# Kernel optimization log

Hardware: AMD Instinct MI355X
Metric: run time of the kernel (lower is better)

The kernel has to match this reference:

```python
import jax, jax.numpy as jnp
import numpy as np

def setup_inputs() -> dict:
    key = jax.random.key(0)
    k1, k2, k3, k4 = jax.random.split(key, 4)
    B, S, E, H = 4, 4096, 1024, 64
    x = jax.random.normal(k1, (B, S, E), dtype=jnp.float32)
    scale = E ** -0.5  # keep activations well-scaled like trained Linear weights
    Wq = jax.random.normal(k2, (E, H), dtype=jnp.float32) * scale
    Wk = jax.random.normal(k3, (E, H), dtype=jnp.float32) * scale
    Wv = jax.random.normal(k4, (E, H), dtype=jnp.float32) * scale
    return {"x": x, "Wq": Wq, "Wk": Wk, "Wv": Wv}

def reference(x, Wq, Wk, Wv):
    # x: [B, S, E]; W*: [E, H]
    B, S, E = x.shape
    H = Wq.shape[1]
    q = jnp.einsum('bse,eh->bsh', x, Wq)
    k = jnp.einsum('bse,eh->bsh', x, Wk)
    v = jnp.einsum('bse,eh->bsh', x, Wv)
    att = jnp.einsum('bqh,bkh->bqk', q, k) * (H ** -0.5)  # [B, S, S]
    causal = jnp.tril(jnp.ones((S, S), dtype=bool))
    att = jnp.where(causal, att, -jnp.inf)
    att = jax.nn.softmax(att, axis=-1)
    # dropout p=0.0 (eval-mode): identity
    return jnp.einsum('bqk,bkh->bqh', att, v)
```

## Files before the change

### kernel.cpp

```cpp
#include <hip/hip_runtime.h>


using short8 = __attribute__((ext_vector_type(8))) short;
using f32x4  = __attribute__((ext_vector_type(4))) float;

#define MFMA16(A, B, C) __builtin_amdgcn_mfma_f32_16x16x32_bf16((A), (B), (C), 0, 0, 0)

typedef const __attribute__((address_space(1))) void* gas_ptr;
typedef __attribute__((address_space(3))) void*       las_ptr;

__device__ __forceinline__ void gload16(const void* g, void* l) {
    __builtin_amdgcn_global_load_lds((gas_ptr)g, (las_ptr)l, 16, 0, 0);
}

__device__ __forceinline__ unsigned short f2bf(float f) {
    unsigned u = __builtin_bit_cast(unsigned, f);
    u += 0x7fffu + ((u >> 16) & 1u);
    return (unsigned short)(u >> 16);
}
__device__ __forceinline__ float bf2f(unsigned short u) {
    unsigned v = ((unsigned)u) << 16;
    return __builtin_bit_cast(float, v);
}

__device__ __forceinline__ float exp2_fast(float x) {
#if __has_builtin(__builtin_amdgcn_exp2f)
    return __builtin_amdgcn_exp2f(x);
#else
    float r;
    asm("v_exp_f32 %0, %1" : "=v"(r) : "v"(x));
    return r;
#endif
}

__global__ __launch_bounds__(256) void transpose_w(
    const float* __restrict__ Wq,
    const float* __restrict__ Wk,
    const float* __restrict__ Wv,
    unsigned short* __restrict__ Ws)
{
    int o = blockIdx.x * 256 + threadIdx.x;
    if (o < 196608) {
        int j    = o & 7;
        int l    = (o >> 3) & 63;
        int g    = (o >> 9) & 7;
        int rem  = o >> 12;
        int mt   = rem % 3;
        int sk   = rem / 3;
        int c    = g >> 2, nt = g & 3;
        int quad = l >> 4, n  = l & 15;
        int e    = sk * 64 + c * 32 + quad * 8 + j;
        int h    = nt * 16 + n;
        const float* W = (mt == 0) ? Wq : (mt == 1) ? Wk : Wv;
        Ws[o] = f2bf(W[e * 64 + h]);
    }
}

__global__ __launch_bounds__(256, 3) void proj_all(
    const float* __restrict__ x,
    const unsigned short* __restrict__ Ws,
    unsigned short* __restrict__ Qo,
    unsigned short* __restrict__ Ko,
    unsigned short* __restrict__ Vto)
{
    const int m0   = blockIdx.x * 32;
    const int tid  = threadIdx.x;
    const int lane = tid & 63;
    const int ch   = tid >> 6;
    const int quad = lane >> 4;
    const int n    = lane & 15;

    __shared__ __align__(16) float xs[2][8][64][4];

    const f32x4 zero4 = {0.f, 0.f, 0.f, 0.f};
    f32x4 acc[3][2];
    #pragma unroll
    for (int mt = 0; mt < 3; ++mt)
        #pragma unroll
        for (int rg = 0; rg < 2; ++rg) acc[mt][rg] = zero4;

    auto stage = [&](int t, int p) {
        int k0 = t * 64;
        #pragma unroll
        for (int it = 0; it < 2; ++it) {
            int i     = ch + 4 * it;
            int chunk = n ^ (quad << 2);
            gload16(x + (size_t)(m0 + 4 * i + quad) * 1024 + k0 + chunk * 4,
                    &xs[p][i][0][0]);
        }
    };

    stage(0, 0);
    __syncthreads();

    int p = 0;
    for (int t = 0; t < 16; ++t) {
        if (t < 15) stage(t + 1, p ^ 1);

        const unsigned short* wp = Ws + (((size_t)t * 24) << 9) + (size_t)lane * 8;
        short8 w0[3], w1[3];
        #pragma unroll
        for (int mt = 0; mt < 3; ++mt) {
            w0[mt] = *(const short8*)(wp + ((size_t)(mt * 8 + ch)     << 9));
            w1[mt] = *(const short8*)(wp + ((size_t)(mt * 8 + 4 + ch) << 9));
        }

        #pragma unroll
        for (int rg = 0; rg < 2; ++rg) {
            int sub = n & 3, s = sub << 2;
            const float* xp = &xs[p][rg * 4 + (n >> 2)][0][0] + sub * 64;
            f32x4 u0 = *(const f32x4*)(xp + (((2 * quad)     ^ s) << 2));
            f32x4 u1 = *(const f32x4*)(xp + (((2 * quad + 1) ^ s) << 2));
            f32x4 u2 = *(const f32x4*)(xp + (((8 + 2 * quad) ^ s) << 2));
            f32x4 u3 = *(const f32x4*)(xp + (((9 + 2 * quad) ^ s) << 2));
            short8 a0, a1;
            #pragma unroll
            for (int j = 0; j < 4; ++j) {
                a0[j]     = (short)f2bf(u0[j]);
                a0[4 + j] = (short)f2bf(u1[j]);
                a1[j]     = (short)f2bf(u2[j]);
                a1[4 + j] = (short)f2bf(u3[j]);
            }
            #pragma unroll
            for (int mt = 0; mt < 3; ++mt) {
                acc[mt][rg] = MFMA16(a0, w0[mt], acc[mt][rg]);
                acc[mt][rg] = MFMA16(a1, w1[mt], acc[mt][rg]);
            }
        }

        __syncthreads();
        p ^= 1;
    }

    const int h = ch * 16 + n;
    #pragma unroll
    for (int rg = 0; rg < 2; ++rg) {
        #pragma unroll
        for (int r = 0; r < 4; ++r) {
            int m = m0 + rg * 16 + quad * 4 + r;
            Qo[(size_t)m * 64 + h] = f2bf(acc[0][rg][r]);
            Ko[(size_t)m * 64 + h] = f2bf(acc[1][rg][r]);
            int b = m >> 12, s2 = m & 4095;
            Vto[((size_t)(b * 80 + h)) * 4096 + s2] = f2bf(acc[2][rg][r]);
        }
    }
}

template <int SPLIT>
__device__ __forceinline__ void attn_body(
    const unsigned short* __restrict__ Q,
    const unsigned short* __restrict__ K,
    const unsigned short* __restrict__ Vt,
    float* __restrict__ dst,
    int b, int r0, int kt0, int kt1)
{
    const int tid  = threadIdx.x;
    const int lane = tid & 63;
    const int wv   = tid >> 6;
    const int quad = lane >> 4;
    const int n    = lane & 15;
    const int ktmask = r0 >> 6;

    __shared__ __align__(16) short kf[2][8][64][8];
    __shared__ __align__(16) short vf[2][8][64][8];
    __shared__ __align__(16) unsigned short pbuf[4][32][72];

    short8 qa[2][2];
    #pragma unroll
    for (int rg = 0; rg < 2; ++rg) {
        const unsigned short* qp =
            Q + (size_t)(b * 4096 + r0 + wv * 32 + rg * 16 + n) * 64 + quad * 8;
        #pragma unroll
        for (int j = 0; j < 8; ++j) {
            qa[rg][0][j] = (short)f2bf(bf2f(qp[j])      * 0.18033688f);
            qa[rg][1][j] = (short)f2bf(bf2f(qp[32 + j]) * 0.18033688f);
        }
    }

    const f32x4 zero4 = {0.f, 0.f, 0.f, 0.f};
    f32x4 oacc[2][4];
    float lacc[2][4];
    #pragma unroll
    for (int rg = 0; rg < 2; ++rg)
        #pragma unroll
        for (int nt = 0; nt < 4; ++nt) { oacc[rg][nt] = zero4; lacc[rg][nt] = 0.f; }

    const unsigned short* kbase = K  + ((size_t)b * 4096 + n) * 64 + quad * 8;
    const unsigned short* vbase = Vt + ((size_t)b * 80 + n) * 4096 + quad * 8;

    auto stage = [&](int kt, int p) {
        #pragma unroll
        for (int it = 0; it < 4; ++it) {
            int f = wv + 4 * it;
            if (f < 8) {
                int c = f >> 2, nt = f & 3;
                gload16(kbase + (size_t)(kt * 64 + nt * 16) * 64 + c * 32, &kf[p][f][0][0]);
            } else {
                int pnl = f - 8;
                int nt = pnl >> 1, c = pnl & 1;
                gload16(vbase + (size_t)nt * 16 * 4096 + kt * 64 + c * 32, &vf[p][pnl][0][0]);
            }
        }
    };

    int p = 0;
    stage(kt0, 0);
    __syncthreads();

    for (int kt = kt0; kt <= kt1; ++kt) {
        if (kt < kt1) stage(kt + 1, p ^ 1);

        f32x4 sacc[2][4];
        #pragma unroll
        for (int rg = 0; rg < 2; ++rg)
            #pragma unroll
            for (int nt = 0; nt < 4; ++nt) sacc[rg][nt] = zero4;

        #pragma unroll
        for (int nt = 0; nt < 4; ++nt) {
            short8 ka = *(const short8*)(&kf[p][nt][lane][0]);
            short8 kb = *(const short8*)(&kf[p][4 + nt][lane][0]);
            #pragma unroll
            for (int rg = 0; rg < 2; ++rg) {
                sacc[rg][nt] = MFMA16(qa[rg][0], ka, sacc[rg][nt]);
                sacc[rg][nt] = MFMA16(qa[rg][1], kb, sacc[rg][nt]);
            }
        }

        if (kt >= ktmask) {
            #pragma unroll
            for (int rg = 0; rg < 2; ++rg) {
                int qg = r0 + wv * 32 + rg * 16 + quad * 4;
                #pragma unroll
                for (int nt = 0; nt < 4; ++nt)
                    #pragma unroll
                    for (int r = 0; r < 4; ++r) {
                        int key = kt * 64 + nt * 16 + n;
                        if (key > qg + r) sacc[rg][nt][r] = -1e30f;
                    }
            }
        }

        #pragma unroll
        for (int rg = 0; rg < 2; ++rg)
            #pragma unroll
            for (int r = 0; r < 4; ++r) {
                float rs = 0.f;
                #pragma unroll
                for (int nt = 0; nt < 4; ++nt) {
                    unsigned short pv = f2bf(exp2_fast(sacc[rg][nt][r]));
                    pbuf[wv][rg * 16 + quad * 4 + r][nt * 16 + n] = pv;
                    rs += bf2f(pv);
                }
                lacc[rg][r] += rs;
            }

        short8 pa[2][2];
        #pragma unroll
        for (int rg = 0; rg < 2; ++rg) {
            pa[rg][0] = *(const short8*)(&pbuf[wv][rg * 16 + n][quad * 8]);
            pa[rg][1] = *(const short8*)(&pbuf[wv][rg * 16 + n][32 + quad * 8]);
        }
        #pragma unroll
        for (int nt = 0; nt < 4; ++nt) {
            short8 va = *(const short8*)(&vf[p][2 * nt][lane][0]);
            short8 vb = *(const short8*)(&vf[p][2 * nt + 1][lane][0]);
            #pragma unroll
            for (int rg = 0; rg < 2; ++rg) {
                oacc[rg][nt] = MFMA16(pa[rg][0], va, oacc[rg][nt]);
                oacc[rg][nt] = MFMA16(pa[rg][1], vb, oacc[rg][nt]);
            }
        }

        __syncthreads();
        p ^= 1;
    }

    #pragma unroll
    for (int rg = 0; rg < 2; ++rg)
        #pragma unroll
        for (int r = 0; r < 4; ++r) {
            float v = lacc[rg][r];
            v += __shfl_xor(v, 1);
            v += __shfl_xor(v, 2);
            v += __shfl_xor(v, 4);
            v += __shfl_xor(v, 8);
            lacc[rg][r] = v;
        }

    if (SPLIT) {
        #pragma unroll
        for (int rg = 0; rg < 2; ++rg)
            #pragma unroll
            for (int r = 0; r < 4; ++r) {
                int row = wv * 32 + rg * 16 + quad * 4 + r;
                #pragma unroll
                for (int nt = 0; nt < 4; ++nt)
                    dst[row * 64 + nt * 16 + n] = oacc[rg][nt][r];
                if (n == 0) dst[8192 + row] = lacc[rg][r];
            }
    } else {
        #pragma unroll
        for (int rg = 0; rg < 2; ++rg)
            #pragma unroll
            for (int r = 0; r < 4; ++r) {
                float inv = 1.f / lacc[rg][r];
                int q = r0 + wv * 32 + rg * 16 + quad * 4 + r;
                #pragma unroll
                for (int nt = 0; nt < 4; ++nt)
                    dst[(size_t)(b * 4096 + q) * 64 + nt * 16 + n] = oacc[rg][nt][r] * inv;
            }
    }
}

__global__ __launch_bounds__(256, 3) void attn_part(
    const unsigned short* __restrict__ Q,
    const unsigned short* __restrict__ K,
    const unsigned short* __restrict__ Vt,
    float* __restrict__ Part)
{
    int id = blockIdx.x;
    int b  = id & 3;
    int t  = 143 - (id >> 2);
    int g  = 0;
    while (2 * (g + 1) * (g + 2) <= t) ++g;
    int u  = t - 2 * g * (g + 1);
    int qt = 4 * g + u / (g + 1);
    int c  = u - (u / (g + 1)) * (g + 1);

    int r0  = qt * 128;
    int kt0 = c * 8;
    int kt1 = min(kt0 + 7, 2 * qt + 1);

    float* dst = Part + (size_t)(b * 144 + t) * 8320;
    attn_body<1>(Q, K, Vt, dst, b, r0, kt0, kt1);
}

__global__ __launch_bounds__(256, 3) void attn_mono(
    const unsigned short* __restrict__ Q,
    const unsigned short* __restrict__ K,
    const unsigned short* __restrict__ Vt,
    float* __restrict__ out)
{
    int id = blockIdx.x;
    int qt = 31 - (id >> 2);
    int b  = id & 3;
    attn_body<0>(Q, K, Vt, out, b, qt * 128, 0, 2 * qt + 1);
}

__global__ __launch_bounds__(256) void combine(
    const float* __restrict__ Part, float* __restrict__ out)
{
    int id    = blockIdx.x;
    int slice = id & 7;
    int bq    = id >> 3;
    int b     = bq & 3;
    int qt    = bq >> 2;
    int g     = qt >> 2;
    int nc    = g + 1;
    int t0    = 2 * g * (g + 1) + (qt & 3) * (g + 1);
    const float* P0 = Part + (size_t)(b * 144 + t0) * 8320;

    int tid = threadIdx.x;

    __shared__ float invden[16];
    if (tid < 16) {
        float d[8] = {0, 0, 0, 0, 0, 0, 0, 0};
        #pragma unroll 8
        for (int c = 0; c < 8; ++c)
            if (c < nc) d[c] = P0[c * 8320 + 8192 + slice * 16 + tid];
        invden[tid] = 1.f / (((d[0] + d[1]) + (d[2] + d[3])) +
                             ((d[4] + d[5]) + (d[6] + d[7])));
    }

    float acc[4] = {0, 0, 0, 0};
    const float* Pe = P0 + slice * 1024 + tid;
    for (int c = 0; c < nc; ++c) {
        const float* Pc = Pe + (size_t)c * 8320;
        #pragma unroll
        for (int j = 0; j < 4; ++j)
            acc[j] += Pc[j * 256];
    }

    __syncthreads();
    #pragma unroll
    for (int j = 0; j < 4; ++j) {
        int e   = j * 256 + tid;
        int row = e >> 6;
        out[((size_t)b * 4096 + qt * 128 + slice * 16) * 64 + (size_t)e]
            = acc[j] * invden[row];
    }
}

extern "C" void kernel_launch(void* const* d_in, const int* in_sizes, int n_in,
                              void* d_out, int out_size, void* d_ws, size_t ws_size,
                              hipStream_t stream) {
    const float* x  = (const float*)d_in[0];
    const float* Wq = (const float*)d_in[1];
    const float* Wk = (const float*)d_in[2];
    const float* Wv = (const float*)d_in[3];
    float* outp = (float*)d_out;
    unsigned short* ws = (unsigned short*)d_ws;

    unsigned short* Qw  = ws;
    unsigned short* Kw  = ws + 1048576;
    unsigned short* Vtw = ws + 2097152;
    unsigned short* Wsp = ws + 3407872;

    size_t part_off = ((size_t)3604480 * 2 + 255) & ~(size_t)255;
    size_t need     = part_off + (size_t)4 * 144 * 8320 * 4;
    float* Part = (float*)((char*)d_ws + part_off);

    transpose_w<<<dim3(768), dim3(256), 0, stream>>>(Wq, Wk, Wv, Wsp);
    proj_all<<<dim3(512), dim3(256), 0, stream>>>(x, Wsp, Qw, Kw, Vtw);

    if (ws_size >= need) {
        attn_part<<<dim3(576), dim3(256), 0, stream>>>(Qw, Kw, Vtw, Part);
        combine<<<dim3(1024), dim3(256), 0, stream>>>(Part, outp);
    } else {
        attn_mono<<<dim3(128), dim3(256), 0, stream>>>(Qw, Kw, Vtw, outp);
    }
}
```

Measured before the change: 141.8 us.

## Load x directly into registers in projection, dropping LDS staging and barriers

The projection kernel no longer stages x tiles through shared memory with async global-to-LDS loads and per-iteration __syncthreads. Each lane now loads its own fp32 x fragments straight into registers, double-buffered across a fully unrolled K loop, with a sched_barrier to order loads ahead of compute. This removes LDS traffic and block synchronization but raises register pressure and may give less coalesced global access. Separately, the attention softmax row sum now accumulates the fp32 exponentials rather than the bf16-rounded values, which saves one conversion per element but slightly changes numerics.

```diff
diff --git a/kernel.cpp b/kernel.cpp
--- a/kernel.cpp
+++ b/kernel.cpp
@@ -70,8 +70,6 @@
     const int quad = lane >> 4;
     const int n    = lane & 15;
 
-    __shared__ __align__(16) float xs[2][8][64][4];
-
     const f32x4 zero4 = {0.f, 0.f, 0.f, 0.f};
     f32x4 acc[3][2];
     #pragma unroll
@@ -79,47 +77,40 @@
         #pragma unroll
         for (int rg = 0; rg < 2; ++rg) acc[mt][rg] = zero4;
 
-    auto stage = [&](int t, int p) {
-        int k0 = t * 64;
-        #pragma unroll
-        for (int it = 0; it < 2; ++it) {
-            int i     = ch + 4 * it;
-            int chunk = n ^ (quad << 2);
-            gload16(x + (size_t)(m0 + 4 * i + quad) * 1024 + k0 + chunk * 4,
-                    &xs[p][i][0][0]);
-        }
+    const float* xr0 = x + (size_t)(m0 + n) * 1024 + 8 * quad;
+    const float* xr1 = x + (size_t)(m0 + 16 + n) * 1024 + 8 * quad;
+    const unsigned short* wl = Ws + (size_t)lane * 8;
+
+    auto xload = [&](int t, f32x4 (&u)[2][4]) {
+        const float* p0 = xr0 + t * 64;
+        const float* p1 = xr1 + t * 64;
+        u[0][0] = *(const f32x4*)(p0);
+        u[0][1] = *(const f32x4*)(p0 + 4);
+        u[0][2] = *(const f32x4*)(p0 + 32);
+        u[0][3] = *(const f32x4*)(p0 + 36);
+        u[1][0] = *(const f32x4*)(p1);
+        u[1][1] = *(const f32x4*)(p1 + 4);
+        u[1][2] = *(const f32x4*)(p1 + 32);
+        u[1][3] = *(const f32x4*)(p1 + 36);
     };
-
-    stage(0, 0);
-    __syncthreads();
-
-    int p = 0;
-    for (int t = 0; t < 16; ++t) {
-        if (t < 15) stage(t + 1, p ^ 1);
-
-        const unsigned short* wp = Ws + (((size_t)t * 24) << 9) + (size_t)lane * 8;
-        short8 w0[3], w1[3];
+    auto wload = [&](int t, short8 (&w0)[3], short8 (&w1)[3]) {
+        const unsigned short* wp = wl + (((size_t)t * 24) << 9);
         #pragma unroll
         for (int mt = 0; mt < 3; ++mt) {
             w0[mt] = *(const short8*)(wp + ((size_t)(mt * 8 + ch)     << 9));
             w1[mt] = *(const short8*)(wp + ((size_t)(mt * 8 + 4 + ch) << 9));
         }
-
+    };
+    auto compute = [&](f32x4 (&u)[2][4], short8 (&w0)[3], short8 (&w1)[3]) {
         #pragma unroll
         for (int rg = 0; rg < 2; ++rg) {
-            int sub = n & 3, s = sub << 2;
-            const float* xp = &xs[p][rg * 4 + (n >> 2)][0][0] + sub * 64;
-            f32x4 u0 = *(const f32x4*)(xp + (((2 * quad)     ^ s) << 2));
-            f32x4 u1 = *(const f32x4*)(xp + (((2 * quad + 1) ^ s) << 2));
-            f32x4 u2 = *(const f32x4*)(xp + (((8 + 2 * quad) ^ s) << 2));
-            f32x4 u3 = *(const f32x4*)(xp + (((9 + 2 * quad) ^ s) << 2));
             short8 a0, a1;
             #pragma unroll
             for (int j = 0; j < 4; ++j) {
-                a0[j]     = (short)f2bf(u0[j]);
-                a0[4 + j] = (short)f2bf(u1[j]);
-                a1[j]     = (short)f2bf(u2[j]);
-                a1[4 + j] = (short)f2bf(u3[j]);
+                a0[j]     = (short)f2bf(u[rg][0][j]);
+                a0[4 + j] = (short)f2bf(u[rg][1][j]);
+                a1[j]     = (short)f2bf(u[rg][2][j]);
+                a1[4 + j] = (short)f2bf(u[rg][3][j]);
             }
             #pragma unroll
             for (int mt = 0; mt < 3; ++mt) {
@@ -127,9 +118,20 @@
                 acc[mt][rg] = MFMA16(a1, w1[mt], acc[mt][rg]);
             }
         }
-
-        __syncthreads();
-        p ^= 1;
+    };
+
+    f32x4 uA[2][4], uB[2][4];
+    short8 w0[3], w1[3];
+    xload(0, uA);
+
+    #pragma unroll
+    for (int t = 0; t < 16; ++t) {
+        wload(t, w0, w1);
+        if (t < 15) {
+            if (t & 1) xload(t + 1, uA); else xload(t + 1, uB);
+        }
+        __builtin_amdgcn_sched_barrier(0);
+        if (t & 1) compute(uB, w0, w1); else compute(uA, w0, w1);
     }
 
     const int h = ch * 16 + n;
@@ -248,9 +250,9 @@
                 float rs = 0.f;
                 #pragma unroll
                 for (int nt = 0; nt < 4; ++nt) {
-                    unsigned short pv = f2bf(exp2_fast(sacc[rg][nt][r]));
-                    pbuf[wv][rg * 16 + quad * 4 + r][nt * 16 + n] = pv;
-                    rs += bf2f(pv);
+                    float pf = exp2_fast(sacc[rg][nt][r]);
+                    pbuf[wv][rg * 16 + quad * 4 + r][nt * 16 + n] = f2bf(pf);
+                    rs += pf;
                 }
                 lacc[rg][r] += rs;
             }
```

New measurement: 156.2 us. +10.2%, slower.
